# Performance work log

Hardware: AMD Instinct MI355X
Metric: run time of the kernel (lower is better)

## Reference

```python
import jax, jax.numpy as jnp
import numpy as np

D_MODEL = 256
N_LAYERS = 2
EXPAND = 2
D_INNER = EXPAND * D_MODEL  # 512
D_STATE = 16
D_CONV = 4
DT_RANK = max(1, D_MODEL // 16)  # 16


def _selective_scan(x, dt, B, C, A, D):
    # x, dt: [b, l, d]   B, C: [b, l, n]   A: [d, n]   D: [d]
    dA = jnp.exp(jnp.einsum('bld,dn->bldn', dt, A))          # discretized state matrix
    dBx = jnp.einsum('bld,bln,bld->bldn', dt, B, x)           # dt * B * u

    def step(h, inp):
        dA_t, dBx_t, C_t = inp                                 # [b,d,n],[b,d,n],[b,n]
        h = dA_t * h + dBx_t
        y = jnp.einsum('bdn,bn->bd', h, C_t)
        return h, y

    h0 = jnp.zeros((x.shape[0], A.shape[0], A.shape[1]), x.dtype)
    _, ys = jax.lax.scan(step, h0, (jnp.moveaxis(dA, 1, 0),
                                    jnp.moveaxis(dBx, 1, 0),
                                    jnp.moveaxis(C, 1, 0)))
    return jnp.moveaxis(ys, 0, 1) + x * D                      # [b, l, d]


def _mamba_block(z, in_w, conv_w, conv_b, xp_w, dt_w, dt_b, A_log, Dp, out_w):
    b, l, _ = z.shape
    xz = z @ in_w.T                                            # [b, l, 2*d_inner]
    x, gate = jnp.split(xz, 2, axis=-1)
    # causal depthwise conv1d over time
    xt = jnp.transpose(x, (0, 2, 1))                            # [b, d_inner, l]
    xt = jax.lax.conv_general_dilated(
        xt, conv_w[:, None, :], window_strides=(1,),
        padding=[(D_CONV - 1, 0)], feature_group_count=D_INNER)
    x = jax.nn.silu(jnp.transpose(xt, (0, 2, 1)) + conv_b)      # [b, l, d_inner]
    x_dbl = x @ xp_w.T                                          # [b, l, dt_rank + 2*d_state]
    dt, Bm, Cm = jnp.split(x_dbl, [DT_RANK, DT_RANK + D_STATE], axis=-1)
    dt = jax.nn.softplus(dt @ dt_w.T + dt_b)                    # [b, l, d_inner]
    A = -jnp.exp(A_log)                                         # [d_inner, d_state]
    y = _selective_scan(x, dt, Bm, Cm, A, Dp)
    y = y * jax.nn.silu(gate)
    return y @ out_w.T                                          # [b, l, d_model]


def setup_inputs() -> dict:
    key = jax.random.key(0)
    ks = jax.random.split(key, 9)
    B, L = 2, 4096
    z = jax.random.normal(ks[0], (B, L, D_MODEL), jnp.float32)
    s = 0.02
    in_proj_w = jax.random.normal(ks[1], (N_LAYERS, 2 * D_INNER, D_MODEL), jnp.float32) * s
    conv_w = jax.random.normal(ks[2], (N_LAYERS, D_INNER, D_CONV), jnp.float32) * 0.2
    conv_b = jnp.zeros((N_LAYERS, D_INNER), jnp.float32)
    x_proj_w = jax.random.normal(ks[3], (N_LAYERS, DT_RANK + 2 * D_STATE, D_INNER), jnp.float32) * s
    dt_proj_w = jax.random.normal(ks[4], (N_LAYERS, D_INNER, DT_RANK), jnp.float32) * 0.1
    dt_proj_b = jax.random.uniform(ks[5], (N_LAYERS, D_INNER), jnp.float32, -4.0, -2.0)
    A_log = jnp.log(jnp.broadcast_to(jnp.arange(1, D_STATE + 1, dtype=jnp.float32),
                                     (N_LAYERS, D_INNER, D_STATE)))
    D_param = jnp.ones((N_LAYERS, D_INNER), jnp.float32)
    out_proj_w = jax.random.normal(ks[6], (N_LAYERS, D_MODEL, D_INNER), jnp.float32) * s
    return {"z": z, "in_proj_w": in_proj_w, "conv_w": conv_w, "conv_b": conv_b,
            "x_proj_w": x_proj_w, "dt_proj_w": dt_proj_w, "dt_proj_b": dt_proj_b,
            "A_log": A_log, "D_param": D_param, "out_proj_w": out_proj_w}


def reference(z, in_proj_w, conv_w, conv_b, x_proj_w, dt_proj_w, dt_proj_b,
              A_log, D_param, out_proj_w):
    for i in range(N_LAYERS):
        z = _mamba_block(z, in_proj_w[i], conv_w[i], conv_b[i], x_proj_w[i],
                         dt_proj_w[i], dt_proj_b[i], A_log[i], D_param[i], out_proj_w[i])
    return z
```

## Files before the change

### kernel.cpp

```cpp
#include <hip/hip_runtime.h>
#include <hip/hip_bf16.h>
#include <cstdint>
#include <cstddef>

#define DM   256
#define DI   512
#define DS   16
#define LSEQ 4096
#define BATCH 2
#define BLROWS (BATCH * LSEQ)
#define NCH  256
#define CLEN 16
#define NSC  16
#define XCP  520

typedef __bf16 bf16x8 __attribute__((ext_vector_type(8)));
typedef float  f32x4  __attribute__((ext_vector_type(4)));
typedef unsigned short u16;
typedef u16 u16x8 __attribute__((ext_vector_type(8)));

__device__ __forceinline__ u16 f2bfu(float f) {
    union { float f; unsigned u; } c; c.f = f;
    unsigned u = c.u;
    return (u16)((u + 0x7fffu + ((u >> 16) & 1u)) >> 16);
}
__device__ __forceinline__ float bfu2f(u16 u) {
    union { unsigned u; float f; } c; c.u = ((unsigned)u) << 16; return c.f;
}
__device__ __forceinline__ float siluf(float v) {
    return v * (1.0f / (1.0f + __expf(-v)));
}
__device__ __forceinline__ void gload_lds16(const void* g, void* l) {
    __builtin_amdgcn_global_load_lds(
        (const __attribute__((address_space(1))) unsigned int*)g,
        (__attribute__((address_space(3))) unsigned int*)l, 16, 0, 0);
}

#define N_INW  (2*1024*256)
#define N_OUTW (2*256*512)
#define N_XPW  (2*64*512)
#define N_Z    (BLROWS*DM)
__global__ __launch_bounds__(256) void cast_all_k(
    const float* __restrict__ in_w, const float* __restrict__ out_w,
    const float* __restrict__ xp_w, const float* __restrict__ z,
    u16* __restrict__ inw_bf, u16* __restrict__ outw_bf,
    u16* __restrict__ xpw_bf, u16* __restrict__ z_bf) {
    int i = blockIdx.x * 256 + threadIdx.x;
    if (i < N_INW) {
        inw_bf[i] = f2bfu(in_w[i]);
    } else if (i < N_INW + N_OUTW) {
        int j = i - N_INW;
        outw_bf[j] = f2bfu(out_w[j]);
    } else if (i < N_INW + N_OUTW + N_XPW) {
        int j = i - (N_INW + N_OUTW);
        int k = j & 511, o = (j >> 9) & 63, l = j >> 15;
        xpw_bf[j] = f2bfu((o < 48) ? xp_w[(l * 48 + o) * 512 + k] : 0.0f);
    } else {
        int j = i - (N_INW + N_OUTW + N_XPW);
        z_bf[j] = f2bfu(z[j]);
    }
}

__global__ __launch_bounds__(256) void gemm_in_k(
    const __bf16* __restrict__ A, const __bf16* __restrict__ B,
    u16* __restrict__ Cb, int M, int N, int K) {
    __shared__ __bf16 As[128 * 32];
    __shared__ __bf16 Bs[128 * 32];
    int tid = threadIdx.x, wave = tid >> 6, lane = tid & 63;
    int bm = blockIdx.x * 128, bn = blockIdx.y * 128;
    int wm = (wave & 1) * 64, wn = (wave >> 1) * 64;
    int row = lane & 15, q = lane >> 4;
    int srow = lane >> 2, sseg = lane & 3;
    f32x4 acc[4][4] = {};
    for (int k0 = 0; k0 < K; k0 += 32) {
        #pragma unroll
        for (int i = 0; i < 2; ++i) {
            int r0 = wave * 32 + i * 16;
            gload_lds16(A + (size_t)(bm + r0 + srow) * K + k0 + sseg * 8, As + r0 * 32);
            gload_lds16(B + (size_t)(bn + r0 + srow) * K + k0 + sseg * 8, Bs + r0 * 32);
        }
        __syncthreads();
        bf16x8 af[4], bfr[4];
        #pragma unroll
        for (int mi = 0; mi < 4; ++mi)
            af[mi] = *(const bf16x8*)&As[(wm + mi*16 + row) * 32 + q * 8];
        #pragma unroll
        for (int ni = 0; ni < 4; ++ni)
            bfr[ni] = *(const bf16x8*)&Bs[(wn + ni*16 + row) * 32 + q * 8];
        #pragma unroll
        for (int mi = 0; mi < 4; ++mi)
            #pragma unroll
            for (int ni = 0; ni < 4; ++ni)
                acc[mi][ni] = __builtin_amdgcn_mfma_f32_16x16x32_bf16(
                    af[mi], bfr[ni], acc[mi][ni], 0, 0, 0);
        __syncthreads();
    }
    #pragma unroll
    for (int mi = 0; mi < 4; ++mi)
        #pragma unroll
        for (int r = 0; r < 4; ++r) {
            size_t gr = (size_t)(bm + wm + mi*16 + q*4 + r) * N;
            #pragma unroll
            for (int ni = 0; ni < 4; ++ni)
                Cb[gr + bn + wn + ni*16 + row] = f2bfu(acc[mi][ni][r]);
        }
}

__global__ __launch_bounds__(512, 4) void fused_a_k(
    const u16* __restrict__ xz, const float* __restrict__ cw,
    const float* __restrict__ cb, const __bf16* __restrict__ xpw,
    const float* __restrict__ dtw, const float* __restrict__ dtb,
    const float* __restrict__ Alog,
    u16* __restrict__ xcb, u16* __restrict__ dtob,
    float* __restrict__ BCg, u16* __restrict__ Pb, u16* __restrict__ Sb) {
    __shared__ u16 xc_s[CLEN * XCP];
    __shared__ float xd_h[2][CLEN * 68];
    int tid = threadIdx.x;
    int c = blockIdx.x, b = blockIdx.y;
    int flat = b * NCH + c;
    int bl0 = b * LSEQ + c * CLEN;
    int d = tid;

    {
        float w0 = cw[d*4], w1 = cw[d*4+1], w2 = cw[d*4+2], w3 = cw[d*4+3];
        float bias = cb[d];
        float xm3 = 0.f, xm2 = 0.f, xm1 = 0.f;
        int l0 = c * CLEN;
        if (l0 - 3 >= 0) xm3 = bfu2f(xz[(size_t)(bl0 - 3) * 1024 + d]);
        if (l0 - 2 >= 0) xm2 = bfu2f(xz[(size_t)(bl0 - 2) * 1024 + d]);
        if (l0 - 1 >= 0) xm1 = bfu2f(xz[(size_t)(bl0 - 1) * 1024 + d]);
        #pragma unroll 4
        for (int t = 0; t < CLEN; ++t) {
            float xcur = bfu2f(xz[(size_t)(bl0 + t) * 1024 + d]);
            float acc = fmaf(w0, xm3, fmaf(w1, xm2, fmaf(w2, xm1, fmaf(w3, xcur, bias))));
            float v = siluf(acc);
            u16 vb = f2bfu(v);
            xc_s[t * XCP + d] = vb;
            xcb[(size_t)(bl0 + t) * DI + d] = vb;
            xm3 = xm2; xm2 = xm1; xm1 = xcur;
        }
    }
    __syncthreads();

    {
        int wave = tid >> 6, lane = tid & 63;
        int row = lane & 15, q = lane >> 4;
        int nt = wave & 3, kh = wave >> 2;
        f32x4 acc = {0.f, 0.f, 0.f, 0.f};
        #pragma unroll
        for (int kb = 0; kb < 8; ++kb) {
            int kk = (kh*8 + kb) * 32;
            bf16x8 a = *(const bf16x8*)&xc_s[row * XCP + kk + q*8];
            bf16x8 bb = *(const bf16x8*)(xpw + (size_t)(nt*16 + row) * 512 + kk + q*8);
            acc = __builtin_amdgcn_mfma_f32_16x16x32_bf16(a, bb, acc, 0, 0, 0);
        }
        #pragma unroll
        for (int r = 0; r < 4; ++r)
            xd_h[kh][(q*4 + r) * 68 + nt*16 + row] = acc[r];
    }
    __syncthreads();
    for (int j = tid; j < CLEN * 68; j += 512) xd_h[0][j] += xd_h[1][j];
    __syncthreads();

    {
        int t = tid >> 5, cc = tid & 31;
        BCg[(size_t)flat * (CLEN*32) + tid] = xd_h[0][t*68 + 16 + cc];
    }

    {
        float dtwr[16];
        const f32x4* w4 = (const f32x4*)(dtw + (size_t)d * 16);
        #pragma unroll
        for (int g = 0; g < 4; ++g) { f32x4 v = w4[g];
            dtwr[g*4] = v[0]; dtwr[g*4+1] = v[1]; dtwr[g*4+2] = v[2]; dtwr[g*4+3] = v[3]; }
        float dtbv = dtb[d];
        float Ac[16];
        const f32x4* a4 = (const f32x4*)(Alog + (size_t)d * 16);
        #pragma unroll
        for (int g = 0; g < 4; ++g) { f32x4 v = a4[g];
            #pragma unroll
            for (int j = 0; j < 4; ++j) Ac[g*4+j] = -__expf(v[j]); }
        bool fastp = true;
        #pragma unroll
        for (int n = 1; n < 16; ++n)
            fastp = fastp && (fabsf(Ac[n] - (float)(n+1) * Ac[0])
                              <= 1e-4f * fabsf(Ac[n]));
        float p[16], s[16];
        #pragma unroll
        for (int n = 0; n < 16; ++n) { p[n] = 1.0f; s[n] = 0.0f; }
        for (int t = 0; t < CLEN; ++t) {
            float acc = dtbv;
            #pragma unroll
            for (int r = 0; r < 16; ++r) acc = fmaf(xd_h[0][t*68 + r], dtwr[r], acc);
            float dtraw = (acc > 20.0f) ? acc : logf(1.0f + __expf(acc));
            float dtv = bfu2f(f2bfu(dtraw));
            dtob[(size_t)(bl0 + t) * DI + d] = f2bfu(dtraw);
            float xv = bfu2f(xc_s[t * XCP + d]);
            float dx = dtv * xv;
            float an[16];
            if (fastp) {
                float a0 = __expf(dtv * Ac[0]);
                an[0] = a0;
                #pragma unroll
                for (int n = 1; n < 16; ++n) an[n] = an[n-1] * a0;
            } else {
                #pragma unroll
                for (int n = 0; n < 16; ++n) an[n] = __expf(dtv * Ac[n]);
            }
            #pragma unroll
            for (int n = 0; n < 16; ++n) {
                s[n] = fmaf(an[n], s[n], xd_h[0][t*68 + 16 + n] * dx);
                p[n] *= an[n];
            }
        }
        size_t base = ((size_t)flat * DI + d) * 16;
        u16x8 pv0, pv1, sv0, sv1;
        #pragma unroll
        for (int n = 0; n < 8; ++n) {
            pv0[n] = f2bfu(p[n]);   pv1[n] = f2bfu(p[8+n]);
            sv0[n] = f2bfu(s[n]);   sv1[n] = f2bfu(s[8+n]);
        }
        *(u16x8*)(Pb + base)     = pv0;  *(u16x8*)(Pb + base + 8) = pv1;
        *(u16x8*)(Sb + base)     = sv0;  *(u16x8*)(Sb + base + 8) = sv1;
    }
}

__global__ __launch_bounds__(256) void scan1_k(
    const u16* __restrict__ Pb, const u16* __restrict__ Sb,
    float* __restrict__ Pagg, float* __restrict__ Sagg) {
    int gid = blockIdx.x * 256 + threadIdx.x;
    int scg = gid >> 13, elow = gid & 8191;
    int b = scg >> 4, sc = scg & 15;
    int cbase = b * NCH + sc * 16;
    float h = 0.f, p = 1.f;
    #pragma unroll
    for (int k = 0; k < 16; ++k) {
        size_t a = (size_t)(cbase + k) * 8192 + elow;
        float Pv = bfu2f(Pb[a]), Sv = bfu2f(Sb[a]);
        h = fmaf(Pv, h, Sv);
        p *= Pv;
    }
    Pagg[(size_t)scg * 8192 + elow] = p;
    Sagg[(size_t)scg * 8192 + elow] = h;
}

__global__ __launch_bounds__(256) void scan2_k(
    const u16* __restrict__ Pb, const u16* __restrict__ Sb,
    const float* __restrict__ Pagg, const float* __restrict__ Sagg,
    float* __restrict__ Hg) {
    int gid = blockIdx.x * 256 + threadIdx.x;
    int scg = gid >> 13, elow = gid & 8191;
    int b = scg >> 4, sc = scg & 15;
    int cbase = b * NCH + sc * 16;
    float h = 0.f;
    for (int s2 = 0; s2 < sc; ++s2) {
        size_t ai = (size_t)(b*16 + s2) * 8192 + elow;
        h = fmaf(Pagg[ai], h, Sagg[ai]);
    }
    #pragma unroll
    for (int k = 0; k < 16; ++k) {
        size_t a = (size_t)(cbase + k) * 8192 + elow;
        Hg[a] = h;
        h = fmaf(bfu2f(Pb[a]), h, bfu2f(Sb[a]));
    }
}

__global__ __launch_bounds__(512, 4) void fused_c_k(
    const u16* __restrict__ xcb, const u16* __restrict__ dtob,
    const float* __restrict__ BCg, const float* __restrict__ Hg,
    const float* __restrict__ Alog, const float* __restrict__ Dp,
    const u16* __restrict__ xz, const __bf16* __restrict__ outw,
    u16* __restrict__ Ob, float* __restrict__ Of) {
    __shared__ u16 y_s[CLEN * XCP];
    __shared__ float BCs[CLEN * 32];
    int tid = threadIdx.x;
    int c = blockIdx.x, b = blockIdx.y;
    int flat = b * NCH + c;
    int bl0 = b * LSEQ + c * CLEN;
    int d = tid;

    BCs[tid] = BCg[(size_t)flat * (CLEN*32) + tid];

    float Ac[16], h[16];
    {
        const f32x4* a4 = (const f32x4*)(Alog + (size_t)d * 16);
        const f32x4* h4 = (const f32x4*)(Hg + ((size_t)flat * DI + d) * 16);
        #pragma unroll
        for (int g = 0; g < 4; ++g) {
            f32x4 av = a4[g]; f32x4 hv = h4[g];
            #pragma unroll
            for (int j = 0; j < 4; ++j) { Ac[g*4+j] = -__expf(av[j]); h[g*4+j] = hv[j]; }
        }
    }
    bool fastp = true;
    #pragma unroll
    for (int n = 1; n < 16; ++n)
        fastp = fastp && (fabsf(Ac[n] - (float)(n+1) * Ac[0]) <= 1e-4f * fabsf(Ac[n]));
    float Dv = Dp[d];
    __syncthreads();

    #pragma unroll 4
    for (int t = 0; t < CLEN; ++t) {
        float dtv = bfu2f(dtob[(size_t)(bl0 + t) * DI + d]);
        float xv  = bfu2f(xcb[(size_t)(bl0 + t) * DI + d]);
        float gv  = bfu2f(xz[(size_t)(bl0 + t) * 1024 + DI + d]);
        float dx = dtv * xv;
        float an[16];
        if (fastp) {
            float a0 = __expf(dtv * Ac[0]);
            an[0] = a0;
            #pragma unroll
            for (int n = 1; n < 16; ++n) an[n] = an[n-1] * a0;
        } else {
            #pragma unroll
            for (int n = 0; n < 16; ++n) an[n] = __expf(dtv * Ac[n]);
        }
        float y = 0.f;
        #pragma unroll
        for (int n = 0; n < 16; ++n) {
            h[n] = fmaf(an[n], h[n], BCs[t*32 + n] * dx);
            y = fmaf(h[n], BCs[t*32 + 16 + n], y);
        }
        float yv = fmaf(xv, Dv, y) * siluf(gv);
        y_s[t * XCP + d] = f2bfu(yv);
    }
    __syncthreads();

    {
        int wave = tid >> 6, lane = tid & 63;
        int row = lane & 15, q = lane >> 4;
        f32x4 acc[2] = {};
        #pragma unroll
        for (int kb = 0; kb < 16; ++kb) {
            bf16x8 a = *(const bf16x8*)&y_s[row * XCP + kb*32 + q*8];
            #pragma unroll
            for (int ni = 0; ni < 2; ++ni) {
                bf16x8 bb = *(const bf16x8*)(outw +
                    (size_t)(wave*32 + ni*16 + row) * 512 + kb*32 + q*8);
                acc[ni] = __builtin_amdgcn_mfma_f32_16x16x32_bf16(a, bb, acc[ni], 0, 0, 0);
            }
        }
        #pragma unroll
        for (int r = 0; r < 4; ++r) {
            size_t gr = (size_t)(bl0 + q*4 + r) * DM;
            #pragma unroll
            for (int ni = 0; ni < 2; ++ni) {
                int gc = wave*32 + ni*16 + row;
                if (Ob) Ob[gr + gc] = f2bfu(acc[ni][r]);
                else    Of[gr + gc] = acc[ni][r];
            }
        }
    }
}

extern "C" void kernel_launch(void* const* d_in, const int* in_sizes, int n_in,
                              void* d_out, int out_size, void* d_ws, size_t ws_size,
                              hipStream_t stream) {
    (void)in_sizes; (void)n_in; (void)out_size; (void)ws_size;
    const float* z_in   = (const float*)d_in[0];
    const float* in_w   = (const float*)d_in[1];
    const float* conv_w = (const float*)d_in[2];
    const float* conv_b = (const float*)d_in[3];
    const float* xp_w   = (const float*)d_in[4];
    const float* dt_w   = (const float*)d_in[5];
    const float* dt_b   = (const float*)d_in[6];
    const float* A_log  = (const float*)d_in[7];
    const float* D_par  = (const float*)d_in[8];
    const float* out_w  = (const float*)d_in[9];
    float* outp = (float*)d_out;

    char* p = (char*)d_ws;
    auto alloc = [&](size_t bytes) { char* r = p; p += (bytes + 255) & ~(size_t)255; return r; };
    u16* z_bf    = (u16*)alloc((size_t)BLROWS*DM*2);
    u16* z2_bf   = (u16*)alloc((size_t)BLROWS*DM*2);
    u16* xz_bf   = (u16*)alloc((size_t)BLROWS*1024*2);
    u16* xc_bf   = (u16*)alloc((size_t)BLROWS*DI*2);
    u16* dt_bf   = (u16*)alloc((size_t)BLROWS*DI*2);
    u16* inw_bf  = (u16*)alloc((size_t)2*1024*256*2);
    u16* outw_bf = (u16*)alloc((size_t)2*256*512*2);
    u16* xpw_bf  = (u16*)alloc((size_t)2*64*512*2);
    float* BCg   = (float*)alloc((size_t)BATCH*NCH*CLEN*32*4);
    u16* Pbuf    = (u16*)alloc((size_t)BATCH*NCH*DI*DS*2);
    u16* Sbuf    = (u16*)alloc((size_t)BATCH*NCH*DI*DS*2);
    float* Hbuf  = (float*)alloc((size_t)BATCH*NCH*DI*DS*4);
    float* PaggG = (float*)alloc((size_t)BATCH*NSC*8192*4);
    float* SaggG = (float*)alloc((size_t)BATCH*NSC*8192*4);

    cast_all_k<<<(N_INW + N_OUTW + N_XPW + N_Z)/256, 256, 0, stream>>>(
        in_w, out_w, xp_w, z_in, inw_bf, outw_bf, xpw_bf, z_bf);

    const u16* zcur = z_bf;
    for (int l = 0; l < 2; ++l) {
        gemm_in_k<<<dim3(BLROWS/128, 1024/128), 256, 0, stream>>>(
            (const __bf16*)zcur, (const __bf16*)(inw_bf + (size_t)l*1024*256),
            xz_bf, BLROWS, 1024, 256);
        fused_a_k<<<dim3(NCH, BATCH), 512, 0, stream>>>(
            xz_bf, conv_w + (size_t)l*DI*4, conv_b + (size_t)l*DI,
            (const __bf16*)(xpw_bf + (size_t)l*64*512),
            dt_w + (size_t)l*DI*16, dt_b + (size_t)l*DI,
            A_log + (size_t)l*DI*DS,
            xc_bf, dt_bf, BCg, Pbuf, Sbuf);
        scan1_k<<<BATCH*NSC*8192/256, 256, 0, stream>>>(Pbuf, Sbuf, PaggG, SaggG);
        scan2_k<<<BATCH*NSC*8192/256, 256, 0, stream>>>(Pbuf, Sbuf, PaggG, SaggG, Hbuf);
        fused_c_k<<<dim3(NCH, BATCH), 512, 0, stream>>>(
            xc_bf, dt_bf, BCg, Hbuf,
            A_log + (size_t)l*DI*DS, D_par + (size_t)l*DI,
            xz_bf, (const __bf16*)(outw_bf + (size_t)l*256*512),
            (l == 0) ? z2_bf : nullptr, (l == 1) ? outp : nullptr);
        zcur = z2_bf;
    }
}
```

Baseline: 231.3 us.

## Restructure input GEMM with full-K LDS A tile and store scan states in bf16

The input projection GEMM now loads the whole 64x256 A tile into padded LDS once and reads B fragments straight from global memory. This removes the per-K-step barriers and the global_load_lds staging, and it specialises the kernel to fixed dimensions. Separately, the chunk-prefix states written by scan2 and read by fused_c are stored as bf16 instead of fp32, which halves that traffic at the cost of precision in the carried hidden state.

```diff
diff --git a/kernel.cpp b/kernel.cpp
--- a/kernel.cpp
+++ b/kernel.cpp
@@ -13,6 +13,7 @@
 #define CLEN 16
 #define NSC  16
 #define XCP  520
+#define ASP  264
 
 typedef __bf16 bf16x8 __attribute__((ext_vector_type(8)));
 typedef float  f32x4  __attribute__((ext_vector_type(4)));
@@ -29,11 +30,6 @@
 }
 __device__ __forceinline__ float siluf(float v) {
     return v * (1.0f / (1.0f + __expf(-v)));
-}
-__device__ __forceinline__ void gload_lds16(const void* g, void* l) {
-    __builtin_amdgcn_global_load_lds(
-        (const __attribute__((address_space(1))) unsigned int*)g,
-        (__attribute__((address_space(3))) unsigned int*)l, 16, 0, 0);
 }
 
 #define N_INW  (2*1024*256)
@@ -61,48 +57,49 @@
     }
 }
 
-__global__ __launch_bounds__(256) void gemm_in_k(
+__global__ __launch_bounds__(256, 2) void gemm_in_k(
     const __bf16* __restrict__ A, const __bf16* __restrict__ B,
-    u16* __restrict__ Cb, int M, int N, int K) {
-    __shared__ __bf16 As[128 * 32];
-    __shared__ __bf16 Bs[128 * 32];
+    u16* __restrict__ Cb) {
+    __shared__ u16 As[64 * ASP];
     int tid = threadIdx.x, wave = tid >> 6, lane = tid & 63;
-    int bm = blockIdx.x * 128, bn = blockIdx.y * 128;
-    int wm = (wave & 1) * 64, wn = (wave >> 1) * 64;
+    int bm = blockIdx.x * 64, bn = blockIdx.y * 256 + wave * 64;
     int row = lane & 15, q = lane >> 4;
-    int srow = lane >> 2, sseg = lane & 3;
+
+    {
+        int col = (tid & 31) * 8;
+        #pragma unroll
+        for (int i = 0; i < 8; ++i) {
+            int r = i * 8 + (tid >> 5);
+            u16x8 v = *(const u16x8*)((const u16*)A + (size_t)(bm + r) * 256 + col);
+            *(u16x8*)&As[r * ASP + col] = v;
+        }
+    }
+    __syncthreads();
+
     f32x4 acc[4][4] = {};
-    for (int k0 = 0; k0 < K; k0 += 32) {
-        #pragma unroll
-        for (int i = 0; i < 2; ++i) {
-            int r0 = wave * 32 + i * 16;
-            gload_lds16(A + (size_t)(bm + r0 + srow) * K + k0 + sseg * 8, As + r0 * 32);
-            gload_lds16(B + (size_t)(bn + r0 + srow) * K + k0 + sseg * 8, Bs + r0 * 32);
-        }
-        __syncthreads();
+    for (int k = 0; k < 8; ++k) {
         bf16x8 af[4], bfr[4];
         #pragma unroll
         for (int mi = 0; mi < 4; ++mi)
-            af[mi] = *(const bf16x8*)&As[(wm + mi*16 + row) * 32 + q * 8];
+            af[mi] = *(const bf16x8*)&As[(mi*16 + row) * ASP + k*32 + q*8];
         #pragma unroll
         for (int ni = 0; ni < 4; ++ni)
-            bfr[ni] = *(const bf16x8*)&Bs[(wn + ni*16 + row) * 32 + q * 8];
+            bfr[ni] = *(const bf16x8*)(B + (size_t)(bn + ni*16 + row) * 256 + k*32 + q*8);
         #pragma unroll
         for (int mi = 0; mi < 4; ++mi)
             #pragma unroll
             for (int ni = 0; ni < 4; ++ni)
                 acc[mi][ni] = __builtin_amdgcn_mfma_f32_16x16x32_bf16(
                     af[mi], bfr[ni], acc[mi][ni], 0, 0, 0);
-        __syncthreads();
     }
     #pragma unroll
     for (int mi = 0; mi < 4; ++mi)
         #pragma unroll
         for (int r = 0; r < 4; ++r) {
-            size_t gr = (size_t)(bm + wm + mi*16 + q*4 + r) * N;
+            size_t gr = (size_t)(bm + mi*16 + q*4 + r) * 1024;
             #pragma unroll
             for (int ni = 0; ni < 4; ++ni)
-                Cb[gr + bn + wn + ni*16 + row] = f2bfu(acc[mi][ni][r]);
+                Cb[gr + bn + ni*16 + row] = f2bfu(acc[mi][ni][r]);
         }
 }
 
@@ -247,7 +244,7 @@
 __global__ __launch_bounds__(256) void scan2_k(
     const u16* __restrict__ Pb, const u16* __restrict__ Sb,
     const float* __restrict__ Pagg, const float* __restrict__ Sagg,
-    float* __restrict__ Hg) {
+    u16* __restrict__ Hg) {
     int gid = blockIdx.x * 256 + threadIdx.x;
     int scg = gid >> 13, elow = gid & 8191;
     int b = scg >> 4, sc = scg & 15;
@@ -260,14 +257,14 @@
     #pragma unroll
     for (int k = 0; k < 16; ++k) {
         size_t a = (size_t)(cbase + k) * 8192 + elow;
-        Hg[a] = h;
+        Hg[a] = f2bfu(h);
         h = fmaf(bfu2f(Pb[a]), h, bfu2f(Sb[a]));
     }
 }
 
 __global__ __launch_bounds__(512, 4) void fused_c_k(
     const u16* __restrict__ xcb, const u16* __restrict__ dtob,
-    const float* __restrict__ BCg, const float* __restrict__ Hg,
+    const float* __restrict__ BCg, const u16* __restrict__ Hg,
     const float* __restrict__ Alog, const float* __restrict__ Dp,
     const u16* __restrict__ xz, const __bf16* __restrict__ outw,
     u16* __restrict__ Ob, float* __restrict__ Of) {
@@ -284,13 +281,17 @@
     float Ac[16], h[16];
     {
         const f32x4* a4 = (const f32x4*)(Alog + (size_t)d * 16);
-        const f32x4* h4 = (const f32x4*)(Hg + ((size_t)flat * DI + d) * 16);
+        const u16* h8 = Hg + ((size_t)flat * DI + d) * 16;
+        u16x8 hv0 = *(const u16x8*)h8;
+        u16x8 hv1 = *(const u16x8*)(h8 + 8);
         #pragma unroll
         for (int g = 0; g < 4; ++g) {
-            f32x4 av = a4[g]; f32x4 hv = h4[g];
-            #pragma unroll
-            for (int j = 0; j < 4; ++j) { Ac[g*4+j] = -__expf(av[j]); h[g*4+j] = hv[j]; }
-        }
+            f32x4 av = a4[g];
+            #pragma unroll
+            for (int j = 0; j < 4; ++j) Ac[g*4+j] = -__expf(av[j]);
+        }
+        #pragma unroll
+        for (int n = 0; n < 8; ++n) { h[n] = bfu2f(hv0[n]); h[8+n] = bfu2f(hv1[n]); }
     }
     bool fastp = true;
     #pragma unroll
@@ -382,7 +383,7 @@
     float* BCg   = (float*)alloc((size_t)BATCH*NCH*CLEN*32*4);
     u16* Pbuf    = (u16*)alloc((size_t)BATCH*NCH*DI*DS*2);
     u16* Sbuf    = (u16*)alloc((size_t)BATCH*NCH*DI*DS*2);
-    float* Hbuf  = (float*)alloc((size_t)BATCH*NCH*DI*DS*4);
+    u16* Hbuf    = (u16*)alloc((size_t)BATCH*NCH*DI*DS*2);
     float* PaggG = (float*)alloc((size_t)BATCH*NSC*8192*4);
     float* SaggG = (float*)alloc((size_t)BATCH*NSC*8192*4);
 
@@ -391,9 +392,9 @@
 
     const u16* zcur = z_bf;
     for (int l = 0; l < 2; ++l) {
-        gemm_in_k<<<dim3(BLROWS/128, 1024/128), 256, 0, stream>>>(
+        gemm_in_k<<<dim3(BLROWS/64, 1024/256), 256, 0, stream>>>(
             (const __bf16*)zcur, (const __bf16*)(inw_bf + (size_t)l*1024*256),
-            xz_bf, BLROWS, 1024, 256);
+            xz_bf);
         fused_a_k<<<dim3(NCH, BATCH), 512, 0, stream>>>(
             xz_bf, conv_w + (size_t)l*DI*4, conv_b + (size_t)l*DI,
             (const __bf16*)(xpw_bf + (size_t)l*64*512),
```

Result: no change. 234.5 us (+1.4%).

## Use power-tree decay, closed-form chunk product, bf16 carry states, higher occupancy

Applied to the files above, without the earlier changes.

The per-step decay powers are now built with a shallow power tree instead of a serial multiply chain. The per-chunk decay product is computed in closed form from the summed dt rather than accumulated each step, which frees 16 registers. The inter-chunk carry state buffer is stored as bf16 instead of fp32, halving its write and read traffic. Launch bounds are raised to 6 blocks per SM, and the y reduction is split into four accumulators. The costs are some loss of precision in the carried states and the product, plus more register pressure if the compiler cannot meet the new bound.

```diff
diff --git a/kernel.cpp b/kernel.cpp
--- a/kernel.cpp
+++ b/kernel.cpp
@@ -35,6 +35,13 @@
         (const __attribute__((address_space(1))) unsigned int*)g,
         (__attribute__((address_space(3))) unsigned int*)l, 16, 0, 0);
 }
+
+#define POW_TREE(an, e1)                                                     \
+    {   float e2 = (e1)*(e1), e4 = e2*e2, e8 = e4*e4;                        \
+        an[0]=(e1); an[1]=e2; an[2]=e2*(e1); an[3]=e4; an[4]=e4*(e1);        \
+        an[5]=e4*e2; an[6]=e4*an[2]; an[7]=e8; an[8]=e8*(e1); an[9]=e8*e2;   \
+        an[10]=e8*an[2]; an[11]=e8*e4; an[12]=e8*an[4]; an[13]=e8*an[5];     \
+        an[14]=e8*an[6]; an[15]=e8*e8; }
 
 #define N_INW  (2*1024*256)
 #define N_OUTW (2*256*512)
@@ -106,7 +113,7 @@
         }
 }
 
-__global__ __launch_bounds__(512, 4) void fused_a_k(
+__global__ __launch_bounds__(512, 6) void fused_a_k(
     const u16* __restrict__ xz, const float* __restrict__ cw,
     const float* __restrict__ cb, const __bf16* __restrict__ xpw,
     const float* __restrict__ dtw, const float* __restrict__ dtb,
@@ -174,50 +181,75 @@
         for (int g = 0; g < 4; ++g) { f32x4 v = w4[g];
             dtwr[g*4] = v[0]; dtwr[g*4+1] = v[1]; dtwr[g*4+2] = v[2]; dtwr[g*4+3] = v[3]; }
         float dtbv = dtb[d];
-        float Ac[16];
-        const f32x4* a4 = (const f32x4*)(Alog + (size_t)d * 16);
-        #pragma unroll
-        for (int g = 0; g < 4; ++g) { f32x4 v = a4[g];
-            #pragma unroll
-            for (int j = 0; j < 4; ++j) Ac[g*4+j] = -__expf(v[j]); }
-        bool fastp = true;
-        #pragma unroll
-        for (int n = 1; n < 16; ++n)
-            fastp = fastp && (fabsf(Ac[n] - (float)(n+1) * Ac[0])
-                              <= 1e-4f * fabsf(Ac[n]));
-        float p[16], s[16];
-        #pragma unroll
-        for (int n = 0; n < 16; ++n) { p[n] = 1.0f; s[n] = 0.0f; }
-        for (int t = 0; t < CLEN; ++t) {
-            float acc = dtbv;
-            #pragma unroll
-            for (int r = 0; r < 16; ++r) acc = fmaf(xd_h[0][t*68 + r], dtwr[r], acc);
-            float dtraw = (acc > 20.0f) ? acc : logf(1.0f + __expf(acc));
-            float dtv = bfu2f(f2bfu(dtraw));
-            dtob[(size_t)(bl0 + t) * DI + d] = f2bfu(dtraw);
-            float xv = bfu2f(xc_s[t * XCP + d]);
-            float dx = dtv * xv;
-            float an[16];
-            if (fastp) {
-                float a0 = __expf(dtv * Ac[0]);
-                an[0] = a0;
+        float Ac0; bool fastp = true;
+        {
+            const f32x4* a4 = (const f32x4*)(Alog + (size_t)d * 16);
+            f32x4 v0 = a4[0];
+            Ac0 = -__expf(v0[0]);
+            #pragma unroll
+            for (int g = 0; g < 4; ++g) { f32x4 v = a4[g];
                 #pragma unroll
-                for (int n = 1; n < 16; ++n) an[n] = an[n-1] * a0;
-            } else {
+                for (int j = 0; j < 4; ++j) { int n = g*4 + j; if (n) {
+                    float acn = -__expf(v[j]);
+                    fastp = fastp && (fabsf(acn - (float)(n+1)*Ac0) <= 1e-4f*fabsf(acn));
+                } } }
+        }
+        float s[16];
+        #pragma unroll
+        for (int n = 0; n < 16; ++n) s[n] = 0.f;
+        float Sdt = 0.f;
+        if (fastp) {
+            for (int t = 0; t < CLEN; ++t) {
+                float acc = dtbv;
                 #pragma unroll
-                for (int n = 0; n < 16; ++n) an[n] = __expf(dtv * Ac[n]);
-            }
-            #pragma unroll
-            for (int n = 0; n < 16; ++n) {
-                s[n] = fmaf(an[n], s[n], xd_h[0][t*68 + 16 + n] * dx);
-                p[n] *= an[n];
-            }
+                for (int r = 0; r < 16; ++r) acc = fmaf(xd_h[0][t*68 + r], dtwr[r], acc);
+                float dtraw = (acc > 20.0f) ? acc : logf(1.0f + __expf(acc));
+                u16 dtu = f2bfu(dtraw);
+                dtob[(size_t)(bl0 + t) * DI + d] = dtu;
+                float dtv = bfu2f(dtu);
+                float xv = bfu2f(xc_s[t * XCP + d]);
+                float dx = dtv * xv;
+                Sdt += dtv;
+                float e1 = __expf(dtv * Ac0);
+                float an[16];
+                POW_TREE(an, e1)
+                #pragma unroll
+                for (int n = 0; n < 16; ++n)
+                    s[n] = fmaf(an[n], s[n], xd_h[0][t*68 + 16 + n] * dx);
+            }
+        } else {
+            for (int t = 0; t < CLEN; ++t) {
+                float acc = dtbv;
+                #pragma unroll
+                for (int r = 0; r < 16; ++r) acc = fmaf(xd_h[0][t*68 + r], dtwr[r], acc);
+                float dtraw = (acc > 20.0f) ? acc : logf(1.0f + __expf(acc));
+                u16 dtu = f2bfu(dtraw);
+                dtob[(size_t)(bl0 + t) * DI + d] = dtu;
+                float dtv = bfu2f(dtu);
+                float xv = bfu2f(xc_s[t * XCP + d]);
+                float dx = dtv * xv;
+                Sdt += dtv;
+                #pragma unroll
+                for (int n = 0; n < 16; ++n) {
+                    float an = __expf(dtv * -__expf(Alog[(size_t)d*16 + n]));
+                    s[n] = fmaf(an, s[n], xd_h[0][t*68 + 16 + n] * dx);
+                }
+            }
+        }
+        float pw[16];
+        if (fastp) {
+            float E1 = __expf(Ac0 * Sdt);
+            POW_TREE(pw, E1)
+        } else {
+            #pragma unroll
+            for (int n = 0; n < 16; ++n)
+                pw[n] = __expf(-__expf(Alog[(size_t)d*16 + n]) * Sdt);
         }
         size_t base = ((size_t)flat * DI + d) * 16;
         u16x8 pv0, pv1, sv0, sv1;
         #pragma unroll
         for (int n = 0; n < 8; ++n) {
-            pv0[n] = f2bfu(p[n]);   pv1[n] = f2bfu(p[8+n]);
+            pv0[n] = f2bfu(pw[n]);  pv1[n] = f2bfu(pw[8+n]);
             sv0[n] = f2bfu(s[n]);   sv1[n] = f2bfu(s[8+n]);
         }
         *(u16x8*)(Pb + base)     = pv0;  *(u16x8*)(Pb + base + 8) = pv1;
@@ -247,7 +279,7 @@
 __global__ __launch_bounds__(256) void scan2_k(
     const u16* __restrict__ Pb, const u16* __restrict__ Sb,
     const float* __restrict__ Pagg, const float* __restrict__ Sagg,
-    float* __restrict__ Hg) {
+    u16* __restrict__ Hg) {
     int gid = blockIdx.x * 256 + threadIdx.x;
     int scg = gid >> 13, elow = gid & 8191;
     int b = scg >> 4, sc = scg & 15;
@@ -260,14 +292,14 @@
     #pragma unroll
     for (int k = 0; k < 16; ++k) {
         size_t a = (size_t)(cbase + k) * 8192 + elow;
-        Hg[a] = h;
+        Hg[a] = f2bfu(h);
         h = fmaf(bfu2f(Pb[a]), h, bfu2f(Sb[a]));
     }
 }
 
-__global__ __launch_bounds__(512, 4) void fused_c_k(
+__global__ __launch_bounds__(512, 6) void fused_c_k(
     const u16* __restrict__ xcb, const u16* __restrict__ dtob,
-    const float* __restrict__ BCg, const float* __restrict__ Hg,
+    const float* __restrict__ BCg, const u16* __restrict__ Hg,
     const float* __restrict__ Alog, const float* __restrict__ Dp,
     const u16* __restrict__ xz, const __bf16* __restrict__ outw,
     u16* __restrict__ Ob, float* __restrict__ Of) {
@@ -281,48 +313,71 @@
 
     BCs[tid] = BCg[(size_t)flat * (CLEN*32) + tid];
 
-    float Ac[16], h[16];
+    float Ac0; bool fastp = true;
     {
         const f32x4* a4 = (const f32x4*)(Alog + (size_t)d * 16);
-        const f32x4* h4 = (const f32x4*)(Hg + ((size_t)flat * DI + d) * 16);
-        #pragma unroll
-        for (int g = 0; g < 4; ++g) {
-            f32x4 av = a4[g]; f32x4 hv = h4[g];
-            #pragma unroll
-            for (int j = 0; j < 4; ++j) { Ac[g*4+j] = -__expf(av[j]); h[g*4+j] = hv[j]; }
-        }
-    }
-    bool fastp = true;
-    #pragma unroll
-    for (int n = 1; n < 16; ++n)
-        fastp = fastp && (fabsf(Ac[n] - (float)(n+1) * Ac[0]) <= 1e-4f * fabsf(Ac[n]));
+        f32x4 v0 = a4[0];
+        Ac0 = -__expf(v0[0]);
+        #pragma unroll
+        for (int g = 0; g < 4; ++g) { f32x4 v = a4[g];
+            #pragma unroll
+            for (int j = 0; j < 4; ++j) { int n = g*4 + j; if (n) {
+                float acn = -__expf(v[j]);
+                fastp = fastp && (fabsf(acn - (float)(n+1)*Ac0) <= 1e-4f*fabsf(acn));
+            } } }
+    }
+    float h[16];
+    {
+        const u16* h8 = Hg + ((size_t)flat * DI + d) * 16;
+        u16x8 hv0 = *(const u16x8*)h8;
+        u16x8 hv1 = *(const u16x8*)(h8 + 8);
+        #pragma unroll
+        for (int n = 0; n < 8; ++n) { h[n] = bfu2f(hv0[n]); h[8+n] = bfu2f(hv1[n]); }
+    }
     float Dv = Dp[d];
     __syncthreads();
 
-    #pragma unroll 4
-    for (int t = 0; t < CLEN; ++t) {
-        float dtv = bfu2f(dtob[(size_t)(bl0 + t) * DI + d]);
-        float xv  = bfu2f(xcb[(size_t)(bl0 + t) * DI + d]);
-        float gv  = bfu2f(xz[(size_t)(bl0 + t) * 1024 + DI + d]);
-        float dx = dtv * xv;
-        float an[16];
-        if (fastp) {
-            float a0 = __expf(dtv * Ac[0]);
-            an[0] = a0;
-            #pragma unroll
-            for (int n = 1; n < 16; ++n) an[n] = an[n-1] * a0;
-        } else {
-            #pragma unroll
-            for (int n = 0; n < 16; ++n) an[n] = __expf(dtv * Ac[n]);
-        }
-        float y = 0.f;
-        #pragma unroll
-        for (int n = 0; n < 16; ++n) {
-            h[n] = fmaf(an[n], h[n], BCs[t*32 + n] * dx);
-            y = fmaf(h[n], BCs[t*32 + 16 + n], y);
-        }
-        float yv = fmaf(xv, Dv, y) * siluf(gv);
-        y_s[t * XCP + d] = f2bfu(yv);
+    if (fastp) {
+        for (int t = 0; t < CLEN; ++t) {
+            float dtv = bfu2f(dtob[(size_t)(bl0 + t) * DI + d]);
+            float xv  = bfu2f(xcb[(size_t)(bl0 + t) * DI + d]);
+            float gv  = bfu2f(xz[(size_t)(bl0 + t) * 1024 + DI + d]);
+            float dx = dtv * xv;
+            float e1 = __expf(dtv * Ac0);
+            float an[16];
+            POW_TREE(an, e1)
+            float y0 = 0.f, y1 = 0.f, y2 = 0.f, y3 = 0.f;
+            #pragma unroll
+            for (int n = 0; n < 4; ++n) {
+                h[n]    = fmaf(an[n],    h[n],    BCs[t*32 + n]    * dx);
+                h[4+n]  = fmaf(an[4+n],  h[4+n],  BCs[t*32 + 4+n]  * dx);
+                h[8+n]  = fmaf(an[8+n],  h[8+n],  BCs[t*32 + 8+n]  * dx);
+                h[12+n] = fmaf(an[12+n], h[12+n], BCs[t*32 + 12+n] * dx);
+                y0 = fmaf(h[n],    BCs[t*32 + 16 + n],    y0);
+                y1 = fmaf(h[4+n],  BCs[t*32 + 16 + 4+n],  y1);
+                y2 = fmaf(h[8+n],  BCs[t*32 + 16 + 8+n],  y2);
+                y3 = fmaf(h[12+n], BCs[t*32 + 16 + 12+n], y3);
+            }
+            float y = (y0 + y1) + (y2 + y3);
+            float yv = fmaf(xv, Dv, y) * siluf(gv);
+            y_s[t * XCP + d] = f2bfu(yv);
+        }
+    } else {
+        for (int t = 0; t < CLEN; ++t) {
+            float dtv = bfu2f(dtob[(size_t)(bl0 + t) * DI + d]);
+            float xv  = bfu2f(xcb[(size_t)(bl0 + t) * DI + d]);
+            float gv  = bfu2f(xz[(size_t)(bl0 + t) * 1024 + DI + d]);
+            float dx = dtv * xv;
+            float y = 0.f;
+            #pragma unroll
+            for (int n = 0; n < 16; ++n) {
+                float an = __expf(dtv * -__expf(Alog[(size_t)d*16 + n]));
+                h[n] = fmaf(an, h[n], BCs[t*32 + n] * dx);
+                y = fmaf(h[n], BCs[t*32 + 16 + n], y);
+            }
+            float yv = fmaf(xv, Dv, y) * siluf(gv);
+            y_s[t * XCP + d] = f2bfu(yv);
+        }
     }
     __syncthreads();
 
@@ -382,7 +437,7 @@
     float* BCg   = (float*)alloc((size_t)BATCH*NCH*CLEN*32*4);
     u16* Pbuf    = (u16*)alloc((size_t)BATCH*NCH*DI*DS*2);
     u16* Sbuf    = (u16*)alloc((size_t)BATCH*NCH*DI*DS*2);
-    float* Hbuf  = (float*)alloc((size_t)BATCH*NCH*DI*DS*4);
+    u16* Hbuf    = (u16*)alloc((size_t)BATCH*NCH*DI*DS*2);
     float* PaggG = (float*)alloc((size_t)BATCH*NSC*8192*4);
     float* SaggG = (float*)alloc((size_t)BATCH*NSC*8192*4);
 
```

Measured after the change: 234.0 us. Within noise of the previous version (+1.2%).

## Fuse two-pass chunk-state scan into one kernel with shared-memory carry

Applied to the files above, without the earlier changes.

Merges the two inter-chunk scan kernels into a single 1024-thread kernel. Each thread keeps its 16 chunk P/S values in registers, writes its super-chunk aggregate to shared memory, and computes the prefix carry after a barrier. This removes the second read of the bf16 P/S buffers, the global aggregate buffers and one kernel launch per layer. In exchange it uses more registers per thread, needs a block-wide barrier, and launches only 256 blocks of 1024 threads.

```diff
diff --git a/kernel.cpp b/kernel.cpp
--- a/kernel.cpp
+++ b/kernel.cpp
@@ -225,43 +225,34 @@
     }
 }
 
-__global__ __launch_bounds__(256) void scan1_k(
+__global__ __launch_bounds__(1024) void scan12_k(
     const u16* __restrict__ Pb, const u16* __restrict__ Sb,
-    float* __restrict__ Pagg, float* __restrict__ Sagg) {
-    int gid = blockIdx.x * 256 + threadIdx.x;
-    int scg = gid >> 13, elow = gid & 8191;
-    int b = scg >> 4, sc = scg & 15;
+    float* __restrict__ Hg) {
+    __shared__ float pag[NSC][64], sag[NSC][64];
+    int tid = threadIdx.x;
+    int eo = tid & 63, sc = tid >> 6;
+    int elow = blockIdx.x * 64 + eo;
+    int b = blockIdx.y;
     int cbase = b * NCH + sc * 16;
+    float Pr[16], Sr[16];
     float h = 0.f, p = 1.f;
     #pragma unroll
     for (int k = 0; k < 16; ++k) {
         size_t a = (size_t)(cbase + k) * 8192 + elow;
-        float Pv = bfu2f(Pb[a]), Sv = bfu2f(Sb[a]);
-        h = fmaf(Pv, h, Sv);
-        p *= Pv;
-    }
-    Pagg[(size_t)scg * 8192 + elow] = p;
-    Sagg[(size_t)scg * 8192 + elow] = h;
-}
-
-__global__ __launch_bounds__(256) void scan2_k(
-    const u16* __restrict__ Pb, const u16* __restrict__ Sb,
-    const float* __restrict__ Pagg, const float* __restrict__ Sagg,
-    float* __restrict__ Hg) {
-    int gid = blockIdx.x * 256 + threadIdx.x;
-    int scg = gid >> 13, elow = gid & 8191;
-    int b = scg >> 4, sc = scg & 15;
-    int cbase = b * NCH + sc * 16;
-    float h = 0.f;
-    for (int s2 = 0; s2 < sc; ++s2) {
-        size_t ai = (size_t)(b*16 + s2) * 8192 + elow;
-        h = fmaf(Pagg[ai], h, Sagg[ai]);
-    }
+        Pr[k] = bfu2f(Pb[a]); Sr[k] = bfu2f(Sb[a]);
+        h = fmaf(Pr[k], h, Sr[k]);
+        p *= Pr[k];
+    }
+    pag[sc][eo] = p; sag[sc][eo] = h;
+    __syncthreads();
+    float hs = 0.f;
+    for (int s2 = 0; s2 < sc; ++s2)
+        hs = fmaf(pag[s2][eo], hs, sag[s2][eo]);
     #pragma unroll
     for (int k = 0; k < 16; ++k) {
         size_t a = (size_t)(cbase + k) * 8192 + elow;
-        Hg[a] = h;
-        h = fmaf(bfu2f(Pb[a]), h, bfu2f(Sb[a]));
+        Hg[a] = hs;
+        hs = fmaf(Pr[k], hs, Sr[k]);
     }
 }
 
@@ -383,8 +374,6 @@
     u16* Pbuf    = (u16*)alloc((size_t)BATCH*NCH*DI*DS*2);
     u16* Sbuf    = (u16*)alloc((size_t)BATCH*NCH*DI*DS*2);
     float* Hbuf  = (float*)alloc((size_t)BATCH*NCH*DI*DS*4);
-    float* PaggG = (float*)alloc((size_t)BATCH*NSC*8192*4);
-    float* SaggG = (float*)alloc((size_t)BATCH*NSC*8192*4);
 
     cast_all_k<<<(N_INW + N_OUTW + N_XPW + N_Z)/256, 256, 0, stream>>>(
         in_w, out_w, xp_w, z_in, inw_bf, outw_bf, xpw_bf, z_bf);
@@ -400,8 +389,7 @@
             dt_w + (size_t)l*DI*16, dt_b + (size_t)l*DI,
             A_log + (size_t)l*DI*DS,
             xc_bf, dt_bf, BCg, Pbuf, Sbuf);
-        scan1_k<<<BATCH*NSC*8192/256, 256, 0, stream>>>(Pbuf, Sbuf, PaggG, SaggG);
-        scan2_k<<<BATCH*NSC*8192/256, 256, 0, stream>>>(Pbuf, Sbuf, PaggG, SaggG, Hbuf);
+        scan12_k<<<dim3(8192/64, BATCH), 1024, 0, stream>>>(Pbuf, Sbuf, Hbuf);
         fused_c_k<<<dim3(NCH, BATCH), 512, 0, stream>>>(
             xc_bf, dt_bf, BCg, Hbuf,
             A_log + (size_t)l*DI*DS, D_par + (size_t)l*DI,
```

New measurement: 221.9 us. -4.0%, faster.
